# Kernel tuning notes

Hardware: AMD Instinct MI355X
Metric: run time of the kernel (lower is better)

## Reference

```python
import math
import jax, jax.numpy as jnp
import numpy as np

D_MODEL = 1024
N_HEADS = 16
D_K = D_MODEL // N_HEADS
THETA = 10000.0
B, S = 2, 2048


def setup_inputs() -> dict:
    key = jax.random.key(0)
    k1, k2, k3 = jax.random.split(key, 3)
    x = jax.random.normal(k1, (B, S, D_MODEL), dtype=jnp.float32)
    token_positions = jnp.arange(B * S, dtype=jnp.int32).reshape(B, S)
    std_qkv = math.sqrt(2.0 / (D_MODEL + 3 * D_MODEL))
    std_o = math.sqrt(2.0 / (D_MODEL + D_MODEL))
    W_qkv = jax.random.truncated_normal(k2, -3.0, 3.0, (3 * D_MODEL, D_MODEL), dtype=jnp.float32) * std_qkv
    W_o = jax.random.truncated_normal(k3, -3.0, 3.0, (D_MODEL, D_MODEL), dtype=jnp.float32) * std_o
    return {"x": x, "W_qkv": W_qkv, "W_o": W_o, "token_positions": token_positions}


def _rope(x, pos):
    # x: (B, H, S, D_K); pos: (B, S) int
    half = D_K // 2
    inv_freq = 1.0 / (THETA ** (jnp.arange(0, D_K, 2, dtype=jnp.float32) / D_K))  # (half,)
    # pos_extended = pos[:, None, :] -> freqs (B, 1, S, half)
    freqs = pos[:, None, :, None].astype(jnp.float32) * inv_freq
    cos, sin = jnp.cos(freqs), jnp.sin(freqs)
    xr = x.reshape(*x.shape[:-1], half, 2)
    x1, x2 = xr[..., 0], xr[..., 1]
    out = jnp.stack([x1 * cos - x2 * sin, x2 * cos + x1 * sin], axis=-1)
    return out.reshape(x.shape)


def reference(x, W_qkv, W_o, token_positions):
    seq_len = x.shape[-2]
    qkv = jnp.einsum('bsi,oi->bso', x, W_qkv)
    q, k, v = jnp.split(qkv, 3, axis=-1)
    # (B, S, H*D) -> (B, H, S, D)
    def to_heads(t):
        return t.reshape(t.shape[0], t.shape[1], N_HEADS, D_K).transpose(0, 2, 1, 3)
    q, k, v = to_heads(q), to_heads(k), to_heads(v)
    q = _rope(q, token_positions)
    k = _rope(k, token_positions)
    scores = jnp.einsum('bhnd,bhmd->bhnm', q, k) / math.sqrt(D_K)
    causal = jnp.tril(jnp.ones((seq_len, seq_len), dtype=bool))
    scores = jnp.where(causal, scores, -jnp.inf)
    attn = jax.nn.softmax(scores, axis=-1)
    out = jnp.einsum('bhnm,bhmd->bhnd', attn, v)
    out = out.transpose(0, 2, 1, 3).reshape(x.shape[0], seq_len, D_MODEL)
    return jnp.einsum('bsi,oi->bso', out, W_o)
```

## Files before the change

kernel.cpp:

```cpp
#include <hip/hip_runtime.h>
#include <cmath>

typedef __bf16 bf16;
typedef bf16 bf16x4 __attribute__((ext_vector_type(4)));
typedef bf16 bf16x8 __attribute__((ext_vector_type(8)));
typedef float f32x4 __attribute__((ext_vector_type(4)));

#define MFMA16(a, b, c) __builtin_amdgcn_mfma_f32_16x16x32_bf16(a, b, c, 0, 0, 0)

__global__ __launch_bounds__(256) void cvt_f32_bf16(
    const float* __restrict__ in, bf16* __restrict__ out, int n) {
  int i = (blockIdx.x * 256 + threadIdx.x) * 4;
  if (i < n) {
    const f32x4 v = *(const f32x4*)(in + i);
    bf16x4 o = {(bf16)v[0], (bf16)v[1], (bf16)v[2], (bf16)v[3]};
    *(bf16x4*)(out + i) = o;
  }
}

template <int EPI>
__global__ __launch_bounds__(256) void gemm_nt(
    const bf16* __restrict__ A, const bf16* __restrict__ Bm,
    const int* __restrict__ tokpos,
    bf16* __restrict__ out0, bf16* __restrict__ out1, bf16* __restrict__ out2,
    float* __restrict__ outF, int N) {
  __shared__ __align__(16) bf16 As[2][128 * 32];
  __shared__ __align__(16) bf16 Bs[2][128 * 32];
  const int tid = threadIdx.x;
  const int w = tid >> 6, lane = tid & 63, quad = lane >> 4, m16 = lane & 15;
  const int m0 = blockIdx.y * 128, n0 = blockIdx.x * 128;
  const int wm = (w >> 1) * 64, wn = (w & 1) * 64;

  f32x4 acc[4][4] = {};

  const int row0 = tid >> 2, ch = tid & 3;
  const bf16* Ag0 = A + (size_t)(m0 + row0) * 1024 + ch * 8;
  const bf16* Ag1 = A + (size_t)(m0 + 64 + row0) * 1024 + ch * 8;
  const bf16* Bg0 = Bm + (size_t)(n0 + row0) * 1024 + ch * 8;
  const bf16* Bg1 = Bm + (size_t)(n0 + 64 + row0) * 1024 + ch * 8;

  bf16x8 ra0, ra1, rb0, rb1;
  auto LOAD = [&](int k0) {
    ra0 = *(const bf16x8*)(Ag0 + k0);
    ra1 = *(const bf16x8*)(Ag1 + k0);
    rb0 = *(const bf16x8*)(Bg0 + k0);
    rb1 = *(const bf16x8*)(Bg1 + k0);
  };
  auto WRITE = [&](int p) {
    *(bf16x8*)(As[p] + tid * 8) = ra0;
    *(bf16x8*)(As[p] + 2048 + tid * 8) = ra1;
    *(bf16x8*)(Bs[p] + tid * 8) = rb0;
    *(bf16x8*)(Bs[p] + 2048 + tid * 8) = rb1;
  };

  LOAD(0);
  WRITE(0);
  __syncthreads();

  int p = 0;
  for (int k0 = 0; k0 < 1024; k0 += 32) {
    const bool more = (k0 + 32) < 1024;
    if (more) LOAD(k0 + 32);
    bf16x8 af[4], bfr[4];
#pragma unroll
    for (int mi = 0; mi < 4; ++mi)
      af[mi] = *(const bf16x8*)(As[p] + (wm + mi * 16 + m16) * 32 + quad * 8);
#pragma unroll
    for (int ni = 0; ni < 4; ++ni)
      bfr[ni] = *(const bf16x8*)(Bs[p] + (wn + ni * 16 + m16) * 32 + quad * 8);
#pragma unroll
    for (int mi = 0; mi < 4; ++mi)
#pragma unroll
      for (int ni = 0; ni < 4; ++ni)
        acc[mi][ni] = MFMA16(af[mi], bfr[ni], acc[mi][ni]);
    if (more) {
      WRITE(1 - p);
      __syncthreads();
      p ^= 1;
    }
  }

  if constexpr (EPI == 0) {
#pragma unroll
    for (int mi = 0; mi < 4; ++mi) {
      int rowb = m0 + wm + mi * 16 + quad * 4;
#pragma unroll
      for (int r = 0; r < 4; ++r) {
        size_t off = (size_t)(rowb + r) * N + n0 + wn;
#pragma unroll
        for (int ni = 0; ni < 4; ++ni)
          outF[off + ni * 16 + m16] = acc[mi][ni][r];
      }
    }
  } else {
#pragma unroll
    for (int mi = 0; mi < 4; ++mi) {
      int rowb = m0 + wm + mi * 16 + quad * 4;
      int pos4[4];
#pragma unroll
      for (int r = 0; r < 4; ++r) pos4[r] = tokpos[rowb + r];
#pragma unroll
      for (int ni = 0; ni < 4; ++ni) {
        int col = n0 + wn + ni * 16 + m16;
        int sec = col >> 10, f = col & 1023, h = f >> 6, d = f & 63;
        if (sec == 2) {
#pragma unroll
          for (int r = 0; r < 4; ++r) {
            int row = rowb + r;
            int bb = row >> 11, s = row & 2047;
            out2[((size_t)(bb * 16 + h) * 64 + d) * 2048 + s] =
                (bf16)acc[mi][ni][r];
          }
        } else {
          float inv = __expf(-(float)(d & ~1) * (9.2103403719762f / 64.f));
          bf16* dst = sec ? out1 : out0;
          const float sc = sec ? 1.0f : 0.125f;
#pragma unroll
          for (int r = 0; r < 4; ++r) {
            float v = acc[mi][ni][r];
            float vp = __shfl_xor(v, 1);
            float ang = (float)pos4[r] * inv;
            float cs, sn;
            __sincosf(ang, &sn, &cs);
            float ov = (d & 1) ? (v * cs + vp * sn) : (v * cs - vp * sn);
            ov *= sc;
            int row = rowb + r;
            int bb = row >> 11, s = row & 2047;
            dst[((size_t)(bb * 16 + h) * 2048 + s) * 64 + d] = (bf16)ov;
          }
        }
      }
    }
  }
}

__global__ __launch_bounds__(256) void attn_kernel(
    const bf16* __restrict__ Q, const bf16* __restrict__ K,
    const bf16* __restrict__ Vt, bf16* __restrict__ O) {
  __shared__ __align__(16) bf16 KP[64 * 72];
  __shared__ __align__(16) bf16 VP[64 * 72];
  __shared__ __align__(16) bf16 PS[2][4][16 * 72];
  const int tid = threadIdx.x;
  const int w = tid >> 6, lane = tid & 63, quad = lane >> 4, m16 = lane & 15;
  const int bh = blockIdx.x;
  const int j = blockIdx.y;
  const int qtA = j, qtB = 31 - j;
  const int q0A = qtA * 64, q0B = qtB * 64;
  const bf16* Qb = Q + (size_t)bh * 2048 * 64;
  const bf16* Kb = K + (size_t)bh * 2048 * 64;
  const bf16* Vb = Vt + (size_t)bh * 64 * 2048;

  const int ch0 = w * 8, ch1 = (w + 4) * 8;
  const bf16* Kg = Kb + (size_t)lane * 64;
  const bf16* Vg = Vb + (size_t)lane * 2048;
  bf16* Kl = KP + lane * 72;
  bf16* Vl = VP + lane * 72;

  const bf16* qrowA = Qb + (size_t)(q0A + w * 16 + m16) * 64;
  const bf16* qrowB = Qb + (size_t)(q0B + w * 16 + m16) * 64;
  bf16x8 aqA[2], aqB[2];
  aqA[0] = *(const bf16x8*)(qrowA + quad * 8);
  aqA[1] = *(const bf16x8*)(qrowA + 32 + quad * 8);
  aqB[0] = *(const bf16x8*)(qrowB + quad * 8);
  aqB[1] = *(const bf16x8*)(qrowB + 32 + quad * 8);

  bf16x8 rk0 = *(const bf16x8*)(Kg + ch0);
  bf16x8 rk1 = *(const bf16x8*)(Kg + ch1);
  bf16x8 rv0 = *(const bf16x8*)(Vg + ch0);
  bf16x8 rv1 = *(const bf16x8*)(Vg + ch1);
  *(bf16x8*)(Kl + ch0) = rk0;
  *(bf16x8*)(Kl + ch1) = rk1;
  *(bf16x8*)(Vl + ch0) = rv0;
  *(bf16x8*)(Vl + ch1) = rv1;
  __syncthreads();

  f32x4 oA[4] = {}, oB[4] = {};
  float lA[4] = {0.f, 0.f, 0.f, 0.f}, lB[4] = {0.f, 0.f, 0.f, 0.f};

  auto strip = [&](const bf16x8* aq, int qt, int kt, f32x4* o, float* lp,
                   bf16* ps) {
    f32x4 sa[4] = {};
#pragma unroll
    for (int kk = 0; kk < 2; ++kk)
#pragma unroll
      for (int ni = 0; ni < 4; ++ni) {
        bf16x8 bk =
            *(const bf16x8*)(KP + (ni * 16 + m16) * 72 + kk * 32 + quad * 8);
        sa[ni] = MFMA16(aq[kk], bk, sa[ni]);
      }
    const bool diag = (kt == qt);
#pragma unroll
    for (int r = 0; r < 4; ++r) {
      int qrel = w * 16 + quad * 4 + r;
#pragma unroll
      for (int ni = 0; ni < 4; ++ni) {
        float pp = exp2f(fmaf(sa[ni][r], 1.44269504f, -11.5415603f));
        if (diag && (ni * 16 + m16) > qrel) pp = 0.f;
        lp[r] += pp;
        ps[(quad * 4 + r) * 72 + ni * 16 + m16] = (bf16)pp;
      }
    }
    bf16x8 ap[2];
    ap[0] = *(const bf16x8*)(ps + m16 * 72 + quad * 8);
    ap[1] = *(const bf16x8*)(ps + m16 * 72 + 32 + quad * 8);
#pragma unroll
    for (int kk = 0; kk < 2; ++kk)
#pragma unroll
      for (int ng = 0; ng < 4; ++ng) {
        bf16x8 bv =
            *(const bf16x8*)(VP + (ng * 16 + m16) * 72 + kk * 32 + quad * 8);
        o[ng] = MFMA16(ap[kk], bv, o[ng]);
      }
  };

  for (int kt = 0; kt <= qtB; ++kt) {
    const bool more = kt < qtB;
    if (more) {
      rk0 = *(const bf16x8*)(Kg + (size_t)(kt + 1) * 64 * 64 + ch0);
      rk1 = *(const bf16x8*)(Kg + (size_t)(kt + 1) * 64 * 64 + ch1);
      rv0 = *(const bf16x8*)(Vg + (kt + 1) * 64 + ch0);
      rv1 = *(const bf16x8*)(Vg + (kt + 1) * 64 + ch1);
    }
    if (kt <= qtA) {
      strip(aqB, qtB, kt, oB, lB, PS[1][w]);
      strip(aqA, qtA, kt, oA, lA, PS[0][w]);
    } else {
      strip(aqB, qtB, kt, oB, lB, PS[1][w]);
    }
    if (more) {
      __syncthreads();
      *(bf16x8*)(Kl + ch0) = rk0;
      *(bf16x8*)(Kl + ch1) = rk1;
      *(bf16x8*)(Vl + ch0) = rv0;
      *(bf16x8*)(Vl + ch1) = rv1;
      __syncthreads();
    }
  }

  const int b = bh >> 4, h = bh & 15;
  auto epilogue = [&](f32x4* o, float* lp, int q0) {
#pragma unroll
    for (int r = 0; r < 4; ++r) {
      float l = lp[r];
      l += __shfl_xor(l, 1);
      l += __shfl_xor(l, 2);
      l += __shfl_xor(l, 4);
      l += __shfl_xor(l, 8);
      float inv_l = 1.f / l;
      int s = q0 + w * 16 + quad * 4 + r;
      size_t rowoff = (size_t)(b * 2048 + s) * 1024 + h * 64;
#pragma unroll
      for (int ng = 0; ng < 4; ++ng)
        O[rowoff + ng * 16 + m16] = (bf16)(o[ng][r] * inv_l);
    }
  };
  epilogue(oA, lA, q0A);
  epilogue(oB, lB, q0B);
}

extern "C" void kernel_launch(void* const* d_in, const int* in_sizes, int n_in,
                              void* d_out, int out_size, void* d_ws, size_t ws_size,
                              hipStream_t stream) {
  (void)in_sizes; (void)n_in; (void)out_size; (void)ws_size;
  const float* x = (const float*)d_in[0];
  const float* Wqkv = (const float*)d_in[1];
  const float* Wo = (const float*)d_in[2];
  const int* tokpos = (const int*)d_in[3];
  float* out = (float*)d_out;

  const size_t NEL = (size_t)2 * 16 * 2048 * 64;
  bf16* Qws = (bf16*)d_ws;
  bf16* Kws = Qws + NEL;
  bf16* Vtw = Kws + NEL;
  bf16* Ows = Vtw + NEL;
  bf16* xb  = Ows + NEL;
  bf16* Wqkvb = xb + NEL;
  bf16* Wob = Wqkvb + (size_t)3072 * 1024;

  cvt_f32_bf16<<<4096, 256, 0, stream>>>(x, xb, 4 * 1024 * 1024);
  cvt_f32_bf16<<<3072, 256, 0, stream>>>(Wqkv, Wqkvb, 3 * 1024 * 1024);
  cvt_f32_bf16<<<1024, 256, 0, stream>>>(Wo, Wob, 1024 * 1024);

  gemm_nt<1><<<dim3(24, 32), 256, 0, stream>>>(xb, Wqkvb, tokpos, Qws, Kws,
                                               Vtw, nullptr, 3072);
  attn_kernel<<<dim3(32, 16), 256, 0, stream>>>(Qws, Kws, Vtw, Ows);
  gemm_nt<0><<<dim3(8, 32), 256, 0, stream>>>(Ows, Wob, nullptr, nullptr,
                                              nullptr, nullptr, out, 1024);
}
```

Before: 210.2 us.

## Double-buffer K/V tiles in attention, specialize diagonal masking, merge conversion kernels

The attention kernel now keeps two LDS buffers for K and V. The next tile is staged into the idle buffer while the current one is used, so each iteration needs one barrier instead of two. The causal mask is applied only on diagonal tiles through a compile-time template flag, which removes the per-element branch from off-diagonal tiles. The three fp32-to-bf16 conversion launches are merged into a single kernel to save launch overhead. The extra LDS buffers double K/V shared memory, which may lower occupancy.

```diff
diff --git a/kernel.cpp b/kernel.cpp
--- a/kernel.cpp
+++ b/kernel.cpp
@@ -1,5 +1,6 @@
 #include <hip/hip_runtime.h>
 #include <cmath>
+#include <type_traits>
 
 typedef __bf16 bf16;
 typedef bf16 bf16x4 __attribute__((ext_vector_type(4)));
@@ -8,14 +9,23 @@
 
 #define MFMA16(a, b, c) __builtin_amdgcn_mfma_f32_16x16x32_bf16(a, b, c, 0, 0, 0)
 
-__global__ __launch_bounds__(256) void cvt_f32_bf16(
-    const float* __restrict__ in, bf16* __restrict__ out, int n) {
+__global__ __launch_bounds__(256) void cvt_all(
+    const float* __restrict__ x, const float* __restrict__ wqkv,
+    const float* __restrict__ wo, bf16* __restrict__ xb,
+    bf16* __restrict__ wqkvb, bf16* __restrict__ wob) {
   int i = (blockIdx.x * 256 + threadIdx.x) * 4;
-  if (i < n) {
-    const f32x4 v = *(const f32x4*)(in + i);
-    bf16x4 o = {(bf16)v[0], (bf16)v[1], (bf16)v[2], (bf16)v[3]};
-    *(bf16x4*)(out + i) = o;
+  const float* src;
+  bf16* dst;
+  if (i < (4 << 20)) {
+    src = x + i; dst = xb + i;
+  } else if (i < (7 << 20)) {
+    src = wqkv + (i - (4 << 20)); dst = wqkvb + (i - (4 << 20));
+  } else {
+    src = wo + (i - (7 << 20)); dst = wob + (i - (7 << 20));
   }
+  const f32x4 v = *(const f32x4*)src;
+  bf16x4 o = {(bf16)v[0], (bf16)v[1], (bf16)v[2], (bf16)v[3]};
+  *(bf16x4*)dst = o;
 }
 
 template <int EPI>
@@ -137,8 +147,8 @@
 __global__ __launch_bounds__(256) void attn_kernel(
     const bf16* __restrict__ Q, const bf16* __restrict__ K,
     const bf16* __restrict__ Vt, bf16* __restrict__ O) {
-  __shared__ __align__(16) bf16 KP[64 * 72];
-  __shared__ __align__(16) bf16 VP[64 * 72];
+  __shared__ __align__(16) bf16 KP[2][64 * 72];
+  __shared__ __align__(16) bf16 VP[2][64 * 72];
   __shared__ __align__(16) bf16 PS[2][4][16 * 72];
   const int tid = threadIdx.x;
   const int w = tid >> 6, lane = tid & 63, quad = lane >> 4, m16 = lane & 15;
@@ -153,8 +163,6 @@
   const int ch0 = w * 8, ch1 = (w + 4) * 8;
   const bf16* Kg = Kb + (size_t)lane * 64;
   const bf16* Vg = Vb + (size_t)lane * 2048;
-  bf16* Kl = KP + lane * 72;
-  bf16* Vl = VP + lane * 72;
 
   const bf16* qrowA = Qb + (size_t)(q0A + w * 16 + m16) * 64;
   const bf16* qrowB = Qb + (size_t)(q0B + w * 16 + m16) * 64;
@@ -164,38 +172,47 @@
   aqB[0] = *(const bf16x8*)(qrowB + quad * 8);
   aqB[1] = *(const bf16x8*)(qrowB + 32 + quad * 8);
 
-  bf16x8 rk0 = *(const bf16x8*)(Kg + ch0);
-  bf16x8 rk1 = *(const bf16x8*)(Kg + ch1);
-  bf16x8 rv0 = *(const bf16x8*)(Vg + ch0);
-  bf16x8 rv1 = *(const bf16x8*)(Vg + ch1);
-  *(bf16x8*)(Kl + ch0) = rk0;
-  *(bf16x8*)(Kl + ch1) = rk1;
-  *(bf16x8*)(Vl + ch0) = rv0;
-  *(bf16x8*)(Vl + ch1) = rv1;
+  bf16x8 rk0, rk1, rv0, rv1;
+  auto PREFETCH = [&](int kt) {
+    rk0 = *(const bf16x8*)(Kg + (size_t)kt * 64 * 64 + ch0);
+    rk1 = *(const bf16x8*)(Kg + (size_t)kt * 64 * 64 + ch1);
+    rv0 = *(const bf16x8*)(Vg + kt * 64 + ch0);
+    rv1 = *(const bf16x8*)(Vg + kt * 64 + ch1);
+  };
+  auto STAGE = [&](int p) {
+    *(bf16x8*)(KP[p] + lane * 72 + ch0) = rk0;
+    *(bf16x8*)(KP[p] + lane * 72 + ch1) = rk1;
+    *(bf16x8*)(VP[p] + lane * 72 + ch0) = rv0;
+    *(bf16x8*)(VP[p] + lane * 72 + ch1) = rv1;
+  };
+
+  PREFETCH(0);
+  STAGE(0);
   __syncthreads();
 
   f32x4 oA[4] = {}, oB[4] = {};
   float lA[4] = {0.f, 0.f, 0.f, 0.f}, lB[4] = {0.f, 0.f, 0.f, 0.f};
-
-  auto strip = [&](const bf16x8* aq, int qt, int kt, f32x4* o, float* lp,
-                   bf16* ps) {
+  const int qrel = w * 16 + quad * 4;
+
+  auto strip = [&](int p, const bf16x8* aq, f32x4* o, float* lp, bf16* ps,
+                   auto diag_c) {
+    constexpr bool DIAG = decltype(diag_c)::value;
     f32x4 sa[4] = {};
 #pragma unroll
     for (int kk = 0; kk < 2; ++kk)
 #pragma unroll
       for (int ni = 0; ni < 4; ++ni) {
-        bf16x8 bk =
-            *(const bf16x8*)(KP + (ni * 16 + m16) * 72 + kk * 32 + quad * 8);
+        bf16x8 bk = *(const bf16x8*)(KP[p] + (ni * 16 + m16) * 72 + kk * 32 +
+                                     quad * 8);
         sa[ni] = MFMA16(aq[kk], bk, sa[ni]);
       }
-    const bool diag = (kt == qt);
 #pragma unroll
     for (int r = 0; r < 4; ++r) {
-      int qrel = w * 16 + quad * 4 + r;
 #pragma unroll
       for (int ni = 0; ni < 4; ++ni) {
         float pp = exp2f(fmaf(sa[ni][r], 1.44269504f, -11.5415603f));
-        if (diag && (ni * 16 + m16) > qrel) pp = 0.f;
+        if constexpr (DIAG)
+          if ((ni * 16 + m16) > qrel + r) pp = 0.f;
         lp[r] += pp;
         ps[(quad * 4 + r) * 72 + ni * 16 + m16] = (bf16)pp;
       }
@@ -207,33 +224,33 @@
     for (int kk = 0; kk < 2; ++kk)
 #pragma unroll
       for (int ng = 0; ng < 4; ++ng) {
-        bf16x8 bv =
-            *(const bf16x8*)(VP + (ng * 16 + m16) * 72 + kk * 32 + quad * 8);
+        bf16x8 bv = *(const bf16x8*)(VP[p] + (ng * 16 + m16) * 72 + kk * 32 +
+                                     quad * 8);
         o[ng] = MFMA16(ap[kk], bv, o[ng]);
       }
   };
-
+  constexpr std::false_type ND{};
+  constexpr std::true_type DG{};
+
+  int p = 0;
   for (int kt = 0; kt <= qtB; ++kt) {
     const bool more = kt < qtB;
+    if (more) PREFETCH(kt + 1);
+    if (kt < qtA) {
+      strip(p, aqB, oB, lB, PS[1][w], ND);
+      strip(p, aqA, oA, lA, PS[0][w], ND);
+    } else if (kt == qtA) {
+      strip(p, aqB, oB, lB, PS[1][w], ND);
+      strip(p, aqA, oA, lA, PS[0][w], DG);
+    } else if (more) {
+      strip(p, aqB, oB, lB, PS[1][w], ND);
+    } else {
+      strip(p, aqB, oB, lB, PS[1][w], DG);
+    }
     if (more) {
-      rk0 = *(const bf16x8*)(Kg + (size_t)(kt + 1) * 64 * 64 + ch0);
-      rk1 = *(const bf16x8*)(Kg + (size_t)(kt + 1) * 64 * 64 + ch1);
-      rv0 = *(const bf16x8*)(Vg + (kt + 1) * 64 + ch0);
-      rv1 = *(const bf16x8*)(Vg + (kt + 1) * 64 + ch1);
-    }
-    if (kt <= qtA) {
-      strip(aqB, qtB, kt, oB, lB, PS[1][w]);
-      strip(aqA, qtA, kt, oA, lA, PS[0][w]);
-    } else {
-      strip(aqB, qtB, kt, oB, lB, PS[1][w]);
-    }
-    if (more) {
+      STAGE(1 - p);
       __syncthreads();
-      *(bf16x8*)(Kl + ch0) = rk0;
-      *(bf16x8*)(Kl + ch1) = rk1;
-      *(bf16x8*)(Vl + ch0) = rv0;
-      *(bf16x8*)(Vl + ch1) = rv1;
-      __syncthreads();
+      p ^= 1;
     }
   }
 
@@ -277,9 +294,7 @@
   bf16* Wqkvb = xb + NEL;
   bf16* Wob = Wqkvb + (size_t)3072 * 1024;
 
-  cvt_f32_bf16<<<4096, 256, 0, stream>>>(x, xb, 4 * 1024 * 1024);
-  cvt_f32_bf16<<<3072, 256, 0, stream>>>(Wqkv, Wqkvb, 3 * 1024 * 1024);
-  cvt_f32_bf16<<<1024, 256, 0, stream>>>(Wo, Wob, 1024 * 1024);
+  cvt_all<<<8192, 256, 0, stream>>>(x, Wqkv, Wo, xb, Wqkvb, Wob);
 
   gemm_nt<1><<<dim3(24, 32), 256, 0, stream>>>(xb, Wqkvb, tokpos, Qws, Kws,
                                                Vtw, nullptr, 3072);
```

Result: faster. 202.9 us (-3.4%).
